# Performance work log

Measured on AMD Instinct MI355X. Metric: run time of the kernel, lower is better.

The kernel has to match this reference:

```python
import jax, jax.numpy as jnp
import numpy as np

MARGIN = 0.3
N, D = 4096, 512
NUM_CLASSES = 64

def setup_inputs() -> dict:
    key = jax.random.key(0)
    k1, k2, k3 = jax.random.split(key, 3)
    src_feat = jax.random.normal(k1, (N, D), dtype=jnp.float32)
    tgt_feat = jax.random.normal(k2, (N, D), dtype=jnp.float32)
    labels = jax.random.randint(k3, (N,), 0, NUM_CLASSES, dtype=jnp.int64)
    return {"src_feat": src_feat, "tgt_feat": tgt_feat, "labels": labels}

def reference(src_feat, tgt_feat, labels):
    # squared Euclidean distance matrix [n, n]
    e1 = jnp.sum(src_feat * src_feat, axis=1, keepdims=True)   # [n,1]
    e2 = jnp.sum(tgt_feat * tgt_feat, axis=1, keepdims=True).T  # [1,n]
    dist = e1 + e2 - 2.0 * (src_feat @ tgt_feat.T)
    dist = jnp.maximum(dist, 0.0)  # matches dist_mat[dist_mat < 0] = 0
    # same-label mask [n, n]
    mask = labels[:, None] == labels[None, :]
    # hard positive: max dist among same-label cols; hard negative: min among others
    dist_ap = jnp.max(jnp.where(mask, dist, -jnp.inf), axis=1)  # [n]
    dist_an = jnp.min(jnp.where(mask, jnp.inf, dist), axis=1)   # [n]
    # MarginRankingLoss with target y = 1: mean(relu(-(an - ap) + margin))
    loss = jnp.mean(jax.nn.relu(dist_ap - dist_an + MARGIN))
    return loss
```

## Files before the change

### kernel.cpp

```cpp
#include <hip/hip_runtime.h>
#include <hip/hip_bf16.h>
#include <stdint.h>

#define N_PTS 4096
#define DIM 512
#define MARGIN_F 0.3f
#define POS_INF_BITS 0x7f800000

typedef short bf16x8 __attribute__((ext_vector_type(8)));
typedef float f32x4 __attribute__((ext_vector_type(4)));

__device__ __forceinline__ unsigned short f2bf(float f) {
    unsigned int b = __float_as_uint(f);
    b += 0x7FFF + ((b >> 16) & 1);
    return (unsigned short)(b >> 16);
}

__device__ __forceinline__ void async16(const unsigned short* g, unsigned short* l) {
    __builtin_amdgcn_global_load_lds(
        (const __attribute__((address_space(1))) unsigned int*)g,
        (__attribute__((address_space(3))) unsigned int*)l,
        16, 0, 0);
}

__global__ __launch_bounds__(256) void prep_kernel(
    const float* __restrict__ src, const float* __restrict__ tgt,
    unsigned short* __restrict__ src_bf, unsigned short* __restrict__ tgt_bf,
    float* __restrict__ e1, float* __restrict__ e2,
    float* __restrict__ ap, float* __restrict__ an)
{
    const int row  = blockIdx.x * 4 + (threadIdx.x >> 6);
    const int lane = threadIdx.x & 63;

    const float4* s4 = (const float4*)(src + (size_t)row * DIM);
    const float4* t4 = (const float4*)(tgt + (size_t)row * DIM);
    float4 a0 = s4[lane], a1 = s4[lane + 64];
    float4 b0 = t4[lane], b1 = t4[lane + 64];

    ushort4 u;
    ushort4* so = (ushort4*)(src_bf + (size_t)row * DIM);
    ushort4* to = (ushort4*)(tgt_bf + (size_t)row * DIM);
    u.x = f2bf(a0.x); u.y = f2bf(a0.y); u.z = f2bf(a0.z); u.w = f2bf(a0.w); so[lane] = u;
    u.x = f2bf(a1.x); u.y = f2bf(a1.y); u.z = f2bf(a1.z); u.w = f2bf(a1.w); so[lane + 64] = u;
    u.x = f2bf(b0.x); u.y = f2bf(b0.y); u.z = f2bf(b0.z); u.w = f2bf(b0.w); to[lane] = u;
    u.x = f2bf(b1.x); u.y = f2bf(b1.y); u.z = f2bf(b1.z); u.w = f2bf(b1.w); to[lane + 64] = u;

    float s1 = a0.x*a0.x + a0.y*a0.y + a0.z*a0.z + a0.w*a0.w
             + a1.x*a1.x + a1.y*a1.y + a1.z*a1.z + a1.w*a1.w;
    float s2 = b0.x*b0.x + b0.y*b0.y + b0.z*b0.z + b0.w*b0.w
             + b1.x*b1.x + b1.y*b1.y + b1.z*b1.z + b1.w*b1.w;
    for (int off = 32; off; off >>= 1) {
        s1 += __shfl_down(s1, off);
        s2 += __shfl_down(s2, off);
    }
    if (lane == 0) {
        e1[row] = s1;
        e2[row] = s2;
        ap[row] = 0.0f;
        an[row] = __int_as_float(POS_INF_BITS);
    }
}

#define BM 128
#define BN 128
#define BK 32

__global__ __launch_bounds__(256) void dist_kernel(
    const unsigned short* __restrict__ src_bf,
    const unsigned short* __restrict__ tgt_bf,
    const float* __restrict__ e1, const float* __restrict__ e2,
    const int* __restrict__ labels,
    float* __restrict__ ap, float* __restrict__ an)
{
    __shared__ unsigned short As[BM * BK];
    __shared__ unsigned short Bs[BN * BK];
    __shared__ int   li[BM];
    __shared__ int   lj[BN];
    __shared__ float e1s[BM];
    __shared__ float e2s[BN];

    const int i0 = blockIdx.y * BM;
    const int j0 = blockIdx.x * BN;
    const int t = threadIdx.x;
    const int lane = t & 63;
    const int wave = t >> 6;

    if (t < BM) { li[t] = labels[i0 + t]; e1s[t] = e1[i0 + t]; }
    else        { int u = t - BM; lj[u] = labels[j0 + u]; e2s[u] = e2[j0 + u]; }

    const int srow = t >> 2;
    const int scol = ((t & 3) ^ ((srow >> 1) & 3)) * 8;
    const unsigned short* gA0 = src_bf + (size_t)(i0 + srow) * DIM + scol;
    const unsigned short* gA1 = src_bf + (size_t)(i0 + 64 + srow) * DIM + scol;
    const unsigned short* gB0 = tgt_bf + (size_t)(j0 + srow) * DIM + scol;
    const unsigned short* gB1 = tgt_bf + (size_t)(j0 + 64 + srow) * DIM + scol;
    unsigned short* ldsA0 = &As[0] + wave * 512;
    unsigned short* ldsA1 = &As[0] + 2048 + wave * 512;
    unsigned short* ldsB0 = &Bs[0] + wave * 512;
    unsigned short* ldsB1 = &Bs[0] + 2048 + wave * 512;

    const int wm = (wave >> 1) * 64;
    const int wn = (wave & 1) * 64;
    const int fr = lane & 15;
    const int quad = lane >> 4;
    const int fkey = (fr >> 1) & 3;

    f32x4 acc[4][4];
    #pragma unroll
    for (int a = 0; a < 4; a++)
        #pragma unroll
        for (int b = 0; b < 4; b++)
            acc[a][b] = (f32x4){0.f, 0.f, 0.f, 0.f};

    for (int kk = 0; kk < DIM; kk += BK) {
        __syncthreads();
        async16(gA0 + kk, ldsA0);
        async16(gA1 + kk, ldsA1);
        async16(gB0 + kk, ldsB0);
        async16(gB1 + kk, ldsB1);
        __syncthreads();

        bf16x8 af[4], bf[4];
        const int cp = (quad ^ fkey) * 8;
        #pragma unroll
        for (int x = 0; x < 4; x++) {
            af[x] = *(const bf16x8*)&As[(wm + x * 16 + fr) * BK + cp];
            bf[x] = *(const bf16x8*)&Bs[(wn + x * 16 + fr) * BK + cp];
        }
        #pragma unroll
        for (int tm = 0; tm < 4; tm++)
            #pragma unroll
            for (int tn = 0; tn < 4; tn++)
                acc[tm][tn] = __builtin_amdgcn_mfma_f32_16x16x32_bf16(
                    af[tm], bf[tn], acc[tm][tn], 0, 0, 0);
    }

    const float INF = __int_as_float(POS_INF_BITS);
    #pragma unroll
    for (int tm = 0; tm < 4; tm++) {
        #pragma unroll
        for (int r = 0; r < 4; r++) {
            const int rl = wm + tm * 16 + quad * 4 + r;
            const float e1v = e1s[rl];
            const int   liv = li[rl];
            float apv = 0.0f;
            float anv = INF;
            #pragma unroll
            for (int tn = 0; tn < 4; tn++) {
                const int cl = wn + tn * 16 + fr;
                float d = e1v + e2s[cl] - 2.0f * acc[tm][tn][r];
                d = fmaxf(d, 0.0f);
                if (liv == lj[cl]) apv = fmaxf(apv, d);
                else               anv = fminf(anv, d);
            }
            #pragma unroll
            for (int off = 1; off < 16; off <<= 1) {
                apv = fmaxf(apv, __shfl_xor(apv, off));
                anv = fminf(anv, __shfl_xor(anv, off));
            }
            if (fr == 0) {
                atomicMax((int*)&ap[i0 + rl], __float_as_int(apv));
                atomicMin((int*)&an[i0 + rl], __float_as_int(anv));
            }
        }
    }
}

__global__ __launch_bounds__(256) void loss_kernel(
    const float* __restrict__ ap, const float* __restrict__ an,
    float* __restrict__ out)
{
    const int t = threadIdx.x;
    float s = 0.0f;
    for (int i = t; i < N_PTS; i += 256) {
        float v = ap[i] - an[i] + MARGIN_F;
        s += fmaxf(v, 0.0f);
    }
    for (int off = 32; off; off >>= 1) s += __shfl_down(s, off);
    __shared__ float red[4];
    if ((t & 63) == 0) red[t >> 6] = s;
    __syncthreads();
    if (t == 0) out[0] = (red[0] + red[1] + red[2] + red[3]) / (float)N_PTS;
}

extern "C" void kernel_launch(void* const* d_in, const int* in_sizes, int n_in,
                              void* d_out, int out_size, void* d_ws, size_t ws_size,
                              hipStream_t stream) {
    const float* src   = (const float*)d_in[0];
    const float* tgt   = (const float*)d_in[1];
    const int* labels  = (const int*)d_in[2];

    char* ws = (char*)d_ws;
    const size_t featB = (size_t)N_PTS * DIM * sizeof(unsigned short);
    unsigned short* src_bf = (unsigned short*)ws;
    unsigned short* tgt_bf = (unsigned short*)(ws + featB);
    float* e1 = (float*)(ws + 2 * featB);
    float* e2 = e1 + N_PTS;
    float* ap = e2 + N_PTS;
    float* an = ap + N_PTS;

    prep_kernel<<<N_PTS / 4, 256, 0, stream>>>(src, tgt, src_bf, tgt_bf,
                                               e1, e2, ap, an);
    dim3 grid(N_PTS / BN, N_PTS / BM);
    dist_kernel<<<grid, 256, 0, stream>>>(src_bf, tgt_bf, e1, e2, labels,
                                          ap, an);
    loss_kernel<<<1, 256, 0, stream>>>(ap, an, (float*)d_out);
}
```

Before: 111.9 us.

## Replace per-row atomics with partial-result buffer and parallel final reduction

The distance kernel now writes per-wave-column partial hard-positive/negative values into a [N, 64] buffer instead of issuing atomicMax/atomicMin on shared row slots. The loss kernel becomes a 32-block kernel that reduces the 64 partials per row and atomically adds into the output, which prep now zeroes. This removes contended global atomics (32 column blocks hitting each row) and the single-block tail reduction. In exchange it costs extra global traffic for the 2 MB partial buffers and makes the final sum order nondeterministic.

```diff
diff --git a/kernel.cpp b/kernel.cpp
--- a/kernel.cpp
+++ b/kernel.cpp
@@ -27,10 +27,12 @@
     const float* __restrict__ src, const float* __restrict__ tgt,
     unsigned short* __restrict__ src_bf, unsigned short* __restrict__ tgt_bf,
     float* __restrict__ e1, float* __restrict__ e2,
-    float* __restrict__ ap, float* __restrict__ an)
+    float* __restrict__ out)
 {
     const int row  = blockIdx.x * 4 + (threadIdx.x >> 6);
     const int lane = threadIdx.x & 63;
+
+    if (blockIdx.x == 0 && threadIdx.x == 0) out[0] = 0.0f;
 
     const float4* s4 = (const float4*)(src + (size_t)row * DIM);
     const float4* t4 = (const float4*)(tgt + (size_t)row * DIM);
@@ -56,21 +58,20 @@
     if (lane == 0) {
         e1[row] = s1;
         e2[row] = s2;
-        ap[row] = 0.0f;
-        an[row] = __int_as_float(POS_INF_BITS);
     }
 }
 
 #define BM 128
 #define BN 128
 #define BK 32
+#define NPART 64
 
 __global__ __launch_bounds__(256) void dist_kernel(
     const unsigned short* __restrict__ src_bf,
     const unsigned short* __restrict__ tgt_bf,
     const float* __restrict__ e1, const float* __restrict__ e2,
     const int* __restrict__ labels,
-    float* __restrict__ ap, float* __restrict__ an)
+    float* __restrict__ ap_part, float* __restrict__ an_part)
 {
     __shared__ unsigned short As[BM * BK];
     __shared__ unsigned short Bs[BN * BK];
@@ -136,6 +137,7 @@
     }
 
     const float INF = __int_as_float(POS_INF_BITS);
+    const int pcol = blockIdx.x * 2 + (wave & 1);
     #pragma unroll
     for (int tm = 0; tm < 4; tm++) {
         #pragma unroll
@@ -159,28 +161,35 @@
                 anv = fminf(anv, __shfl_xor(anv, off));
             }
             if (fr == 0) {
-                atomicMax((int*)&ap[i0 + rl], __float_as_int(apv));
-                atomicMin((int*)&an[i0 + rl], __float_as_int(anv));
+                ap_part[(size_t)(i0 + rl) * NPART + pcol] = apv;
+                an_part[(size_t)(i0 + rl) * NPART + pcol] = anv;
             }
         }
     }
 }
 
-__global__ __launch_bounds__(256) void loss_kernel(
-    const float* __restrict__ ap, const float* __restrict__ an,
+__global__ __launch_bounds__(128) void loss_kernel(
+    const float* __restrict__ ap_part, const float* __restrict__ an_part,
     float* __restrict__ out)
 {
-    const int t = threadIdx.x;
-    float s = 0.0f;
-    for (int i = t; i < N_PTS; i += 256) {
-        float v = ap[i] - an[i] + MARGIN_F;
-        s += fmaxf(v, 0.0f);
-    }
+    const int row = blockIdx.x * 128 + threadIdx.x;
+    const float4* a4 = (const float4*)(ap_part + (size_t)row * NPART);
+    const float4* n4 = (const float4*)(an_part + (size_t)row * NPART);
+    float apv = 0.0f;
+    float anv = __int_as_float(POS_INF_BITS);
+    #pragma unroll
+    for (int i = 0; i < NPART / 4; i++) {
+        float4 a = a4[i], n = n4[i];
+        apv = fmaxf(apv, fmaxf(fmaxf(a.x, a.y), fmaxf(a.z, a.w)));
+        anv = fminf(anv, fminf(fminf(n.x, n.y), fminf(n.z, n.w)));
+    }
+    float s = fmaxf(apv - anv + MARGIN_F, 0.0f);
     for (int off = 32; off; off >>= 1) s += __shfl_down(s, off);
-    __shared__ float red[4];
-    if ((t & 63) == 0) red[t >> 6] = s;
+    __shared__ float red[2];
+    if ((threadIdx.x & 63) == 0) red[threadIdx.x >> 6] = s;
     __syncthreads();
-    if (t == 0) out[0] = (red[0] + red[1] + red[2] + red[3]) / (float)N_PTS;
+    if (threadIdx.x == 0)
+        atomicAdd(out, (red[0] + red[1]) / (float)N_PTS);
 }
 
 extern "C" void kernel_launch(void* const* d_in, const int* in_sizes, int n_in,
@@ -196,13 +205,13 @@
     unsigned short* tgt_bf = (unsigned short*)(ws + featB);
     float* e1 = (float*)(ws + 2 * featB);
     float* e2 = e1 + N_PTS;
-    float* ap = e2 + N_PTS;
-    float* an = ap + N_PTS;
+    float* ap_part = e2 + N_PTS;
+    float* an_part = ap_part + (size_t)N_PTS * NPART;
 
     prep_kernel<<<N_PTS / 4, 256, 0, stream>>>(src, tgt, src_bf, tgt_bf,
-                                               e1, e2, ap, an);
+                                               e1, e2, (float*)d_out);
     dim3 grid(N_PTS / BN, N_PTS / BM);
     dist_kernel<<<grid, 256, 0, stream>>>(src_bf, tgt_bf, e1, e2, labels,
-                                          ap, an);
-    loss_kernel<<<1, 256, 0, stream>>>(ap, an, (float*)d_out);
-}
+                                          ap_part, an_part);
+    loss_kernel<<<N_PTS / 128, 128, 0, stream>>>(ap_part, an_part, (float*)d_out);
+}
```

New measurement: 107.0 us. 4.4% less time.
